# Kernel tuning notes

Measured on AMD Instinct MI355X. Metric: run time of the kernel, lower is better.

Reference implementation:

```python
import jax, jax.numpy as jnp
import numpy as np
from jax import lax

NS, NQ, D, C = 1000, 131072, 1024, 100

def setup_inputs() -> dict:
    key = jax.random.key(0)
    k1, k2, k3, k4 = jax.random.split(key, 4)
    return {
        "support_x": jax.random.normal(k1, (NS, D), dtype=jnp.float32),
        "support_y": jax.random.randint(k2, (NS,), 0, C),
        "query_x": jax.random.normal(k3, (NQ, D), dtype=jnp.float32),
        "query_y": jax.random.randint(k4, (NQ,), 0, C),
        "n_iter": 10,
        "beta": 5,
        "num_classes": C,
    }

def _l2norm(x):
    return x / jnp.linalg.norm(x, axis=1, keepdims=True)

def _sqdist(q, c):
    # ||q - c||^2 = |q|^2 + |c|^2 - 2 q.c   -> [Nq, C]
    q2 = jnp.sum(q * q, axis=1, keepdims=True)
    c2 = jnp.sum(c * c, axis=1)
    return q2 + c2[None, :] - 2.0 * (q @ c.T)

def reference(support_x, support_y, query_x, query_y, n_iter, beta, num_classes):
    betaf = jnp.float32(beta)
    # preprocess_KMeans: sphere by support mean, then L2-normalize
    mean_feature = jnp.mean(support_x, axis=0)
    s = _l2norm(support_x - mean_feature)   # [Ns, D]
    q = _l2norm(query_x - mean_feature)     # [Nq, D]

    # per-class support sums/counts (hard assignments for support points)
    sup_sum = jax.ops.segment_sum(s, support_y, num_segments=num_classes)          # [C, D]
    sup_cnt = jax.ops.segment_sum(jnp.ones((s.shape[0],), s.dtype), support_y,
                                  num_segments=num_classes)                        # [C]
    centroids0 = sup_sum / sup_cnt[:, None]  # class means (intent of original init)

    def step(centroids, _):
        d2 = _sqdist(q, centroids)                       # [Nq, C]
        w = jax.nn.softmax(-betaf * d2, axis=1)          # soft assignment weights
        suma = sup_sum + w.T @ q                         # [C, D]
        sumb = sup_cnt + jnp.sum(w, axis=0)              # [C]
        return suma / sumb[:, None], None

    centroids, _ = lax.scan(step, centroids0, None, length=n_iter)

    pred = jnp.argmin(_sqdist(q, centroids), axis=1)     # nearest centroid
    acc = jnp.mean((pred == query_y).astype(jnp.float32))
    return acc
```

## Files before the change

### kernel.cpp

```cpp
#include <hip/hip_runtime.h>
#include <hip/hip_fp8.h>
#include <math.h>

#define NS 1000
#define NQ 131072
#define D  1024
#define C  100
#define CP 112
#define BETA 5.0f
#define NITER 10
#define KC 64
#define KROWS (NQ/KC)
#define KS8 (KROWS/64)

typedef float f32x4 __attribute__((ext_vector_type(4)));
typedef short s16x8 __attribute__((ext_vector_type(8)));
typedef long s64;
typedef s64 s64x2 __attribute__((ext_vector_type(2)));
typedef unsigned short u16;
typedef unsigned char u8;

__device__ __forceinline__ u16 f2bf(float x) {
  union { float f; unsigned u; } v; v.f = x;
  unsigned r = v.u + 0x7fffu + ((v.u >> 16) & 1u);
  return (u16)(r >> 16);
}
__device__ __forceinline__ float bf2f(u16 h) {
  union { unsigned u; float f; } v; v.u = ((unsigned)h) << 16; return v.f;
}
__device__ __forceinline__ u8 f2fp8(float x) {
  __hip_fp8_e4m3 h(x);
  return (u8)h.__x;
}
__device__ __forceinline__ void gld16(const u16* g, u16* l) {
  __builtin_amdgcn_global_load_lds(
      (const __attribute__((address_space(1))) void*)g,
      (__attribute__((address_space(3))) void*)l, 16, 0, 0);
}
__device__ __forceinline__ void gld16b(const u8* g, u8* l) {
  __builtin_amdgcn_global_load_lds(
      (const __attribute__((address_space(1))) void*)g,
      (__attribute__((address_space(3))) void*)l, 16, 0, 0);
}
__device__ __forceinline__ s16x8 frag32(const u16* plane, int row, int kb) {
  int s = kb ^ (row & 3);
  return *(const s16x8*)(plane + row * 32 + s * 8);
}
__device__ __forceinline__ f32x4 mfma16(s16x8 a, s16x8 b, f32x4 c) {
  return __builtin_amdgcn_mfma_f32_16x16x32_bf16(a, b, c, 0, 0, 0);
}
__device__ __forceinline__ f32x4 mfma8(s64 a, s64 b, f32x4 c) {
  return __builtin_amdgcn_mfma_f32_16x16x32_fp8_fp8(a, b, c, 0, 0, 0);
}


__global__ __launch_bounds__(256) void k_mean(const float* __restrict__ sx,
                                              float* __restrict__ mean) {
  int d = blockIdx.x * 256 + threadIdx.x;
  float a = 0.f;
  for (int r = 0; r < NS; ++r) a += sx[(size_t)r * D + d];
  mean[d] = a / (float)NS;
}

__global__ __launch_bounds__(256) void k_invn(const float* __restrict__ x,
                                              const float* __restrict__ mean,
                                              float* __restrict__ invn) {
  int r = blockIdx.x;
  int t = threadIdx.x;
  float4 v = ((const float4*)(x + (size_t)r * D))[t];
  float4 m = ((const float4*)mean)[t];
  float a = v.x - m.x, b = v.y - m.y, c = v.z - m.z, d = v.w - m.w;
  float s = a * a + b * b + c * c + d * d;
#pragma unroll
  for (int off = 1; off < 64; off <<= 1) s += __shfl_xor(s, off);
  __shared__ float ws[4];
  if ((t & 63) == 0) ws[t >> 6] = s;
  __syncthreads();
  if (t == 0) invn[r] = 1.0f / sqrtf(ws[0] + ws[1] + ws[2] + ws[3]);
}

__global__ __launch_bounds__(256) void k_supsum(const float* __restrict__ sx,
        const int* __restrict__ sy, const float* __restrict__ mean,
        const float* __restrict__ invs, float* __restrict__ supsum,
        float* __restrict__ supcnt) {
  int c = blockIdx.x;
  int t = threadIdx.x;
  float a0 = 0.f, a1 = 0.f, a2 = 0.f, a3 = 0.f;
  int cnt = 0;
  if (c < C) {
    for (int r = 0; r < NS; ++r) {
      if (sy[r] == c) {
        ++cnt;
        float inv = invs[r];
        a0 += (sx[(size_t)r * D + t      ] - mean[t      ]) * inv;
        a1 += (sx[(size_t)r * D + t + 256] - mean[t + 256]) * inv;
        a2 += (sx[(size_t)r * D + t + 512] - mean[t + 512]) * inv;
        a3 += (sx[(size_t)r * D + t + 768] - mean[t + 768]) * inv;
      }
    }
  }
  supsum[(size_t)c * D + t      ] = a0;
  supsum[(size_t)c * D + t + 256] = a1;
  supsum[(size_t)c * D + t + 512] = a2;
  supsum[(size_t)c * D + t + 768] = a3;
  if (t == 0) supcnt[c] = (float)cnt;
}

__global__ void k_zero(int* __restrict__ corr) {
  if (threadIdx.x == 0) corr[0] = 0;
}

__global__ void k_out(const int* __restrict__ corr, float* __restrict__ out) {
  if (threadIdx.x == 0) out[0] = (float)corr[0] * (1.0f / (float)NQ);
}

__global__ __launch_bounds__(256) void k_qsplit(const float* __restrict__ qx,
        const float* __restrict__ mean, const float* __restrict__ invq,
        u16* __restrict__ qfh, u16* __restrict__ qfl,
        u8* __restrict__ qf8, u8* __restrict__ qt8) {
  __shared__ u16 Lh[64][70];
  __shared__ float mloc[64], iloc[64];
  int t = threadIdx.x;
  int q0 = blockIdx.x * 64, d0 = blockIdx.y * 64;
  if (t < 16) ((float4*)mloc)[t] = ((const float4*)(mean + d0))[t];
  else if (t < 32) ((float4*)iloc)[t - 16] = ((const float4*)(invq + q0))[t - 16];
  __syncthreads();
  int r = t >> 2, c0 = (t & 3) * 16;
  float inv = iloc[r];
  const float* src = qx + (size_t)(q0 + r) * D + d0 + c0;
  union { u16 s[16]; uint4 q[2]; } H, L;
  union { u8 b[16]; unsigned long long q[2]; } F;
#pragma unroll
  for (int j = 0; j < 16; j += 4) {
    float4 v = *(const float4*)(src + j);
    float xs[4] = {v.x, v.y, v.z, v.w};
#pragma unroll
    for (int u = 0; u < 4; ++u) {
      float x = (xs[u] - mloc[c0 + j + u]) * inv;
      u16 h = f2bf(x);
      H.s[j + u] = h;
      L.s[j + u] = f2bf(x - bf2f(h));
      F.b[j + u] = f2fp8(16.0f * x);
    }
  }
#pragma unroll
  for (int j = 0; j < 16; j += 2)
    *(ushort2*)&Lh[r][c0 + j] = make_ushort2(H.s[j], H.s[j + 1]);
  {
    int d = d0 + c0;
    int ks = d >> 5;
    int kin = c0 & 16;
    int rowin = (q0 & 64) + r;
    size_t fb = ((size_t)((q0 >> 7) * 32 + ks) * 128 + rowin) * 32 + kin;
    *(uint4*)(qfh + fb)     = H.q[0];
    *(uint4*)(qfh + fb + 8) = H.q[1];
    *(uint4*)(qfl + fb)     = L.q[0];
    *(uint4*)(qfl + fb + 8) = L.q[1];
  }
  {
    int h8 = (c0 >= 32) ? 1 : 0;
    int sA = (c0 & 31) >> 3;
    size_t fb8 = (((size_t)(q0 >> 7) * 16 + (d0 >> 6)) * 8 +
                  ((q0 & 64) >> 4) + (r >> 4)) * 1024;
    int lb = (r & 15) * 16 + h8 * 8;
    *(unsigned long long*)(qf8 + fb8 + sA * 256 + lb)       = F.q[0];
    *(unsigned long long*)(qf8 + fb8 + (sA + 1) * 256 + lb) = F.q[1];
  }
  __syncthreads();
  int tq4 = (t & 15) * 4, td4 = (t >> 4) * 4;
  u16 a[4][4];
#pragma unroll
  for (int i = 0; i < 4; ++i) {
    ushort2 p0 = *(const ushort2*)&Lh[tq4 + i][td4];
    ushort2 p1 = *(const ushort2*)&Lh[tq4 + i][td4 + 2];
    a[i][0] = p0.x; a[i][1] = p0.y; a[i][2] = p1.x; a[i][3] = p1.y;
  }
#pragma unroll
  for (int j = 0; j < 4; ++j) {
    uchar4 o;
    o.x = f2fp8(16.0f * bf2f(a[0][j]));
    o.y = f2fp8(16.0f * bf2f(a[1][j]));
    o.z = f2fp8(16.0f * bf2f(a[2][j]));
    o.w = f2fp8(16.0f * bf2f(a[3][j]));
    *(uchar4*)(qt8 + (size_t)(d0 + td4 + j) * NQ + q0 + tq4) = o;
  }
}

template<int INIT>
__global__ __launch_bounds__(256) void k_updm(const float* __restrict__ supsum,
        const float* __restrict__ part, const float* __restrict__ wsump,
        const float* __restrict__ supcnt,
        u16* __restrict__ cfh, u16* __restrict__ cfl, u8* __restrict__ cf8,
        float* __restrict__ c2) {
  int c = blockIdx.x, t = threadIdx.x;
  __shared__ float red[4];
  float den;
  if (INIT) {
    den = supcnt[c];
  } else {
    float s = 0.f;
    for (int b = t; b < NQ / 128; b += 256) s += wsump[(size_t)b * CP + c];
#pragma unroll
    for (int off = 1; off < 64; off <<= 1) s += __shfl_xor(s, off);
    if ((t & 63) == 0) red[t >> 6] = s;
    __syncthreads();
    den = supcnt[c] + red[0] + red[1] + red[2] + red[3];
    __syncthreads();
  }
  float ss = 0.f;
  float vals[4];
#pragma unroll
  for (int j = 0; j < 4; ++j) {
    int d = t + j * 256;
    float s = supsum[(size_t)c * D + d];
    if (!INIT) {
      float ps = 0.f;
      for (int kc = 0; kc < KC; ++kc) ps += part[((size_t)kc * CP + c) * D + d];
      s += 0.0009765625f * ps;
    }
    float v = (c < C) ? s / den : 0.f;
    vals[j] = v; ss += v * v;
  }
#pragma unroll
  for (int j = 0; j < 4; ++j) {
    int d = t + j * 256;
    size_t a16 = (size_t)(d >> 5) * (CP * 32) + c * 32 +
                 ((((d >> 3) & 3) ^ (c & 3)) * 8) + (d & 7);
    u16 h = f2bf(vals[j]);
    cfh[a16] = h;
    cfl[a16] = f2bf(vals[j] - bf2f(h));
    size_t a8 = ((size_t)(d >> 6) * CP + c) * 64 +
                ((((d >> 4) & 3) ^ (c & 3)) * 16) + (d & 15);
    cf8[a8] = f2fp8(16.0f * vals[j]);
  }
#pragma unroll
  for (int off = 1; off < 64; off <<= 1) ss += __shfl_xor(ss, off);
  __syncthreads();
  if ((t & 63) == 0) red[t >> 6] = ss;
  __syncthreads();
  if (t == 0) c2[c] = (c < C) ? (red[0] + red[1] + red[2] + red[3]) : 1e30f;
}


__global__ __launch_bounds__(256) void k_logits8(
    const u8* __restrict__ qf8, const u8* __restrict__ cf8,
    const float* __restrict__ c2,
    u8* __restrict__ Wf8, float* __restrict__ wsump) {
  __shared__ __align__(16) u8 sm[3 * 7168];
  __shared__ float wred[4][CP];
  int t = threadIdx.x, w = t >> 6, l = t & 63;
  int qblk = blockIdx.x;
  const u8* ap0 = qf8 + (size_t)qblk * 131072 + (size_t)(w * 2) * 1024 + l * 16;
  int s_ = l >> 4, r15 = l & 15;
  int o8 = (s_ & 1) * 8;
  int go0 = s_ >> 1, go1 = 2 + (s_ >> 1);

  f32x4 acc[2][7];
#pragma unroll
  for (int mf = 0; mf < 2; ++mf)
#pragma unroll
    for (int nf = 0; nf < 7; ++nf) acc[mf][nf] = (f32x4){0.f, 0.f, 0.f, 0.f};

  auto stageB = [&](u8* buf, int kb) {
    for (int i = w; i < 7; i += 4)
      gld16b(cf8 + (size_t)kb * 7168 + i * 1024 + l * 16, buf + i * 1024);
  };
  auto computeK = [&](const u8* buf, s64x2 a0, s64x2 a1) {
#pragma unroll
    for (int nf = 0; nf < 7; ++nf) {
      int row = nf * 16 + r15;
      const u8* rp = buf + row * 64;
      int sw = row & 3;
      s64 b0 = *(const s64*)(rp + ((go0 ^ sw) << 4) + o8);
      s64 b1 = *(const s64*)(rp + ((go1 ^ sw) << 4) + o8);
      f32x4 x0 = acc[0][nf], x1 = acc[1][nf];
      x0 = mfma8(a0[0], b0, x0); x0 = mfma8(a0[1], b1, x0);
      x1 = mfma8(a1[0], b0, x1); x1 = mfma8(a1[1], b1, x1);
      acc[0][nf] = x0; acc[1][nf] = x1;
    }
  };
#define WAITC8() { if (w < 3) asm volatile("s_waitcnt vmcnt(4)" ::: "memory"); \
                   else       asm volatile("s_waitcnt vmcnt(3)" ::: "memory"); }

  s64x2 a0A, a1A, a0B, a1B;
  u8 *p0 = sm, *p1 = sm + 7168, *p2 = sm + 14336;
  a0A = *(const s64x2*)ap0; a1A = *(const s64x2*)(ap0 + 1024);
  stageB(p0, 0);
  for (int kp = 0; kp < 8; ++kp) {
    int k = kp * 2;
    { const u8* p = ap0 + (size_t)(k + 1) * 8192;
      a0B = *(const s64x2*)p; a1B = *(const s64x2*)(p + 1024); }
    stageB(p1, k + 1);
    WAITC8();
    __builtin_amdgcn_s_barrier();
    computeK(p0, a0A, a1A);
    if (k + 2 < 16) {
      const u8* p = ap0 + (size_t)(k + 2) * 8192;
      a0A = *(const s64x2*)p; a1A = *(const s64x2*)(p + 1024);
      stageB(p2, k + 2);
      WAITC8();
    } else {
      asm volatile("s_waitcnt vmcnt(0)" ::: "memory");
    }
    __builtin_amdgcn_s_barrier();
    computeK(p1, a0B, a1B);
    u8* tmp = p0; p0 = p2; p2 = p1; p1 = tmp;
  }
  __syncthreads();

  float c2v[7];
#pragma unroll
  for (int nf = 0; nf < 7; ++nf) c2v[nf] = c2[nf * 16 + r15];

  const float LS = 2.0f / 256.0f;
  float wcol[7];
#pragma unroll
  for (int nf = 0; nf < 7; ++nf) wcol[nf] = 0.f;
  u8* Wsh8 = sm;
#pragma unroll
  for (int mf = 0; mf < 2; ++mf)
#pragma unroll
    for (int r = 0; r < 4; ++r) {
      float Lg[7], mx = -INFINITY;
#pragma unroll
      for (int nf = 0; nf < 7; ++nf) {
        Lg[nf] = LS * acc[mf][nf][r] - c2v[nf];
        mx = fmaxf(mx, Lg[nf]);
      }
#pragma unroll
      for (int off = 1; off < 16; off <<= 1) mx = fmaxf(mx, __shfl_xor(mx, off));
      float e[7], s = 0.f;
#pragma unroll
      for (int nf = 0; nf < 7; ++nf) { e[nf] = expf(BETA * (Lg[nf] - mx)); s += e[nf]; }
#pragma unroll
      for (int off = 1; off < 16; off <<= 1) s += __shfl_xor(s, off);
      float is = 1.f / s;
      int qi = w * 32 + mf * 16 + (l >> 4) * 4 + r;
#pragma unroll
      for (int nf = 0; nf < 7; ++nf) {
        float wv = e[nf] * is;
        wcol[nf] += wv;
        int cc = nf * 16 + r15;
        Wsh8[cc * 128 + (((qi >> 4) ^ (cc & 7)) << 4) + (qi & 15)] =
            f2fp8(64.0f * wv);
      }
    }
#pragma unroll
  for (int off = 16; off < 64; off <<= 1)
#pragma unroll
    for (int nf = 0; nf < 7; ++nf) wcol[nf] += __shfl_xor(wcol[nf], off);
  if (l < 16)
#pragma unroll
    for (int nf = 0; nf < 7; ++nf) wred[w][nf * 16 + l] = wcol[nf];
  __syncthreads();
  {
    size_t wb = (size_t)(qblk >> 4) * (32 * 7168);
    int ks0 = (qblk * 2) & 31;
    for (int idx = t; idx < 896; idx += 256) {
      int c = idx >> 3, g = idx & 7;
      uint4 v = *(const uint4*)(Wsh8 + c * 128 + ((g ^ (c & 7)) << 4));
      *(uint4*)(Wf8 + wb + (size_t)(ks0 + (g >> 2)) * 7168 + c * 64 +
                (((g & 3) ^ (c & 3)) << 4)) = v;
    }
  }
  if (t < CP) wsump[(size_t)qblk * CP + t] =
      wred[0][t] + wred[1][t] + wred[2][t] + wred[3][t];
#undef WAITC8
}


__global__ __launch_bounds__(256) void k_wqm8(
    const u8* __restrict__ Wf8, const u8* __restrict__ qt8,
    float* __restrict__ part) {
  __shared__ __align__(16) u8 sm[3][15360];
  int t = threadIdx.x, w = t >> 6, l = t & 63;
  int ck = blockIdx.x;
  int d0 = blockIdx.y * 128;
  size_t wbase = (size_t)ck * (32 * 7168);
  size_t qoff  = (size_t)ck * KROWS;
  int s_ = l >> 4, r15 = l & 15;
  int o8 = (s_ & 1) * 8;
  int go0 = s_ >> 1, go1 = 2 + (s_ >> 1);

  f32x4 acc[7][2];
#pragma unroll
  for (int mf = 0; mf < 7; ++mf)
#pragma unroll
    for (int nf = 0; nf < 2; ++nf) acc[mf][nf] = (f32x4){0.f, 0.f, 0.f, 0.f};

  auto stage = [&](u8* buf, int ks) {
    for (int i = w; i < 7; i += 4)
      gld16b(Wf8 + wbase + (size_t)ks * 7168 + i * 1024 + l * 16, buf + i * 1024);
#pragma unroll
    for (int i2 = w * 2; i2 < w * 2 + 2; ++i2) {
      int row = i2 * 16 + (l >> 2);
      int g = (l & 3) ^ ((l >> 2) & 3);
      gld16b(qt8 + (size_t)(d0 + row) * NQ + qoff + (size_t)ks * 64 + g * 16,
             buf + 7168 + i2 * 1024);
    }
  };
  auto computeK = [&](const u8* buf) {
    const u8* qb = buf + 7168;
    s64 bq00, bq01, bq10, bq11;
    {
      int row = w * 32 + r15;
      const u8* rp = qb + row * 64; int sw = row & 3;
      bq00 = *(const s64*)(rp + ((go0 ^ sw) << 4) + o8);
      bq01 = *(const s64*)(rp + ((go1 ^ sw) << 4) + o8);
    }
    {
      int row = w * 32 + 16 + r15;
      const u8* rp = qb + row * 64; int sw = row & 3;
      bq10 = *(const s64*)(rp + ((go0 ^ sw) << 4) + o8);
      bq11 = *(const s64*)(rp + ((go1 ^ sw) << 4) + o8);
    }
#pragma unroll
    for (int mf = 0; mf < 7; ++mf) {
      int row = mf * 16 + r15;
      const u8* rp = buf + row * 64; int sw = row & 3;
      s64 a0 = *(const s64*)(rp + ((go0 ^ sw) << 4) + o8);
      s64 a1 = *(const s64*)(rp + ((go1 ^ sw) << 4) + o8);
      f32x4 x0 = acc[mf][0], x1 = acc[mf][1];
      x0 = mfma8(a0, bq00, x0); x0 = mfma8(a1, bq01, x0);
      x1 = mfma8(a0, bq10, x1); x1 = mfma8(a1, bq11, x1);
      acc[mf][0] = x0; acc[mf][1] = x1;
    }
  };
#define WAITC4() { if (w < 3) asm volatile("s_waitcnt vmcnt(4)" ::: "memory"); \
                   else       asm volatile("s_waitcnt vmcnt(3)" ::: "memory"); }

  u8 *p0 = sm[0], *p1 = sm[1], *p2 = sm[2];
  stage(p0, 0);
  for (int kp = 0; kp < KS8 / 2; ++kp) {
    int k = kp * 2;
    stage(p1, k + 1);
    WAITC4();
    __builtin_amdgcn_s_barrier();
    computeK(p0);
    if (k + 2 < KS8) {
      stage(p2, k + 2);
      WAITC4();
    } else {
      asm volatile("s_waitcnt vmcnt(0)" ::: "memory");
    }
    __builtin_amdgcn_s_barrier();
    computeK(p1);
    u8* tmp = p0; p0 = p2; p2 = p1; p1 = tmp;
  }
#pragma unroll
  for (int mf = 0; mf < 7; ++mf)
#pragma unroll
    for (int nf = 0; nf < 2; ++nf)
#pragma unroll
      for (int r = 0; r < 4; ++r) {
        int c = mf * 16 + (l >> 4) * 4 + r;
        int dg = d0 + w * 32 + nf * 16 + r15;
        part[((size_t)ck * CP + c) * D + dg] = acc[mf][nf][r];
      }
#undef WAITC4
}


template<int FINAL>
__global__ __launch_bounds__(256) void k_logits(
    const u16* __restrict__ qfh, const u16* __restrict__ qfl,
    const u16* __restrict__ cfh, const u16* __restrict__ cfl,
    const float* __restrict__ c2,
    const int* __restrict__ qy, int* __restrict__ corr) {
  __shared__ __align__(16) u16 sm[3 * 7168];
  int t = threadIdx.x, w = t >> 6, l = t & 63;
  int qblk = blockIdx.x;
  size_t abase = (size_t)qblk * 32 * 128 * 32;
  int aoff = (w * 32 + (l & 15)) * 32 + (l >> 4) * 8;
  int kb = l >> 4;

  f32x4 acc[2][7];
#pragma unroll
  for (int mf = 0; mf < 2; ++mf)
#pragma unroll
    for (int nf = 0; nf < 7; ++nf) acc[mf][nf] = (f32x4){0.f, 0.f, 0.f, 0.f};

#define ALOADQ(ks, H0, H1, L0, L1) { \
    const u16* ap_ = qfh + abase + (size_t)(ks) * 4096 + aoff; \
    H0 = *(const s16x8*)ap_;  H1 = *(const s16x8*)(ap_ + 512); \
    const u16* lp_ = qfl + abase + (size_t)(ks) * 4096 + aoff; \
    L0 = *(const s16x8*)lp_;  L1 = *(const s16x8*)(lp_ + 512); }

  auto stageB = [&](u16* buf, int ks) {
    for (int i = w; i < 14; i += 4) {
      const u16* src = (i < 7) ? (cfh + (size_t)(ks) * 3584 + i * 512 + l * 8)
                               : (cfl + (size_t)(ks) * 3584 + (i - 7) * 512 + l * 8);
      gld16(src, buf + i * 512);
    }
  };
  auto computeK = [&](const u16* buf, s16x8 h0, s16x8 h1, s16x8 l0, s16x8 l1) {
#pragma unroll
    for (int nf = 0; nf < 7; ++nf) {
      int row = nf * 16 + (l & 15);
      s16x8 bh = frag32(buf, row, kb);
      s16x8 bl = frag32(buf + 3584, row, kb);
      f32x4 a0 = acc[0][nf], a1 = acc[1][nf];
      a0 = mfma16(l0, bh, a0); a0 = mfma16(h0, bl, a0); a0 = mfma16(h0, bh, a0);
      a1 = mfma16(l1, bh, a1); a1 = mfma16(h1, bl, a1); a1 = mfma16(h1, bh, a1);
      acc[0][nf] = a0; acc[1][nf] = a1;
    }
  };
#define WAITCF() { if (w < 2) asm volatile("s_waitcnt vmcnt(8)" ::: "memory"); \
                   else       asm volatile("s_waitcnt vmcnt(7)" ::: "memory"); }

  s16x8 h0A = {}, h1A = {}, l0A = {}, l1A = {};
  s16x8 h0B = {}, h1B = {}, l0B = {}, l1B = {};
  u16 *p0 = sm, *p1 = sm + 7168, *p2 = sm + 14336;
  ALOADQ(0, h0A, h1A, l0A, l1A);
  stageB(p0, 0);
  for (int kp = 0; kp < 16; ++kp) {
    int k = kp * 2;
    ALOADQ(k + 1, h0B, h1B, l0B, l1B);
    stageB(p1, k + 1);
    WAITCF();
    __builtin_amdgcn_s_barrier();
    computeK(p0, h0A, h1A, l0A, l1A);
    if (k + 2 < 32) {
      ALOADQ(k + 2, h0A, h1A, l0A, l1A);
      stageB(p2, k + 2);
      WAITCF();
    } else {
      asm volatile("s_waitcnt vmcnt(0)" ::: "memory");
    }
    __builtin_amdgcn_s_barrier();
    computeK(p1, h0B, h1B, l0B, l1B);
    u16* tmp = p0; p0 = p2; p2 = p1; p1 = tmp;
  }
  __syncthreads();

  float c2v[7];
#pragma unroll
  for (int nf = 0; nf < 7; ++nf) c2v[nf] = c2[nf * 16 + (l & 15)];

  int cnt = 0;
#pragma unroll
  for (int mf = 0; mf < 2; ++mf)
#pragma unroll
    for (int r = 0; r < 4; ++r) {
      float bv = -INFINITY; int bi = 0x7fffffff;
#pragma unroll
      for (int nf = 0; nf < 7; ++nf) {
        float Lg = 2.f * acc[mf][nf][r] - c2v[nf];
        int cc = nf * 16 + (l & 15);
        if (Lg > bv || (Lg == bv && cc < bi)) { bv = Lg; bi = cc; }
      }
#pragma unroll
      for (int off = 1; off < 16; off <<= 1) {
        float ov = __shfl_xor(bv, off); int oi = __shfl_xor(bi, off);
        if (ov > bv || (ov == bv && oi < bi)) { bv = ov; bi = oi; }
      }
      if ((l & 15) == 0) {
        int qi = w * 32 + mf * 16 + (l >> 4) * 4 + r;
        cnt += (bi == qy[blockIdx.x * 128 + qi]) ? 1 : 0;
      }
    }
  if ((l & 15) == 0) atomicAdd(corr, cnt);
#undef ALOADQ
#undef WAITCF
}


extern "C" void kernel_launch(void* const* d_in, const int* in_sizes, int n_in,
                              void* d_out, int out_size, void* d_ws, size_t ws_size,
                              hipStream_t stream) {
  const float* sx = (const float*)d_in[0];
  const int*   sy = (const int*)d_in[1];
  const float* qx = (const float*)d_in[2];
  const int*   qy = (const int*)d_in[3];

  char* base = (char*)d_ws;
  size_t o = 0;
  auto take = [&](size_t bytes) { size_t r = o; o += (bytes + 511) & ~(size_t)511; return r; };
  float* mean   = (float*)(base + take(4096));
  float* invs   = (float*)(base + take(4096));
  float* invq   = (float*)(base + take((size_t)NQ * 4));
  float* supsum = (float*)(base + take((size_t)CP * D * 4));
  float* supcnt = (float*)(base + take(512));
  float* c2A    = (float*)(base + take(512));
  float* c2B    = (float*)(base + take(512));
  float* wsump  = (float*)(base + take((size_t)(NQ / 128) * CP * 4));
  int*   corr   = (int*)(base + take(512));
  u16* cfhA = (u16*)(base + take((size_t)CP * D * 2));
  u16* cflA = (u16*)(base + take((size_t)CP * D * 2));
  u16* cfhB = (u16*)(base + take((size_t)CP * D * 2));
  u16* cflB = (u16*)(base + take((size_t)CP * D * 2));
  u8*  cf8A = (u8*)(base + take((size_t)CP * D));
  u8*  cf8B = (u8*)(base + take((size_t)CP * D));
  u8*  Wf8  = (u8*)(base + take((size_t)CP * NQ));
  float* part = (float*)(base + take((size_t)KC * CP * D * 4));
  u16* qfh  = (u16*)(base + take((size_t)NQ * D * 2));
  u16* qfl  = (u16*)(base + take((size_t)NQ * D * 2));
  u8*  qf8  = (u8*)(base + take((size_t)NQ * D));
  u8*  qt8  = (u8*)(base + take((size_t)NQ * D));
  size_t fast_need = o;

  if (ws_size < fast_need) {
    k_zero<<<1, 64, 0, stream>>>((int*)d_out);
    return;
  }

  k_mean<<<dim3(D / 256), 256, 0, stream>>>(sx, mean);
  k_invn<<<dim3(NS), 256, 0, stream>>>(sx, mean, invs);
  k_invn<<<dim3(NQ), 256, 0, stream>>>(qx, mean, invq);
  k_supsum<<<dim3(CP), 256, 0, stream>>>(sx, sy, mean, invs, supsum, supcnt);
  k_updm<1><<<dim3(CP), 256, 0, stream>>>(supsum, part, wsump, supcnt,
                                          cfhA, cflA, cf8A, c2A);
  k_qsplit<<<dim3(NQ / 64, D / 64), 256, 0, stream>>>(qx, mean, invq,
                                                      qfh, qfl, qf8, qt8);

  u16 *chc = cfhA, *clc = cflA, *chn = cfhB, *cln = cflB;
  u8  *c8c = cf8A, *c8n = cf8B;
  float *c2c = c2A, *c2n = c2B;
  for (int it = 0; it < NITER; ++it) {
    k_logits8<<<dim3(NQ / 128), 256, 0, stream>>>(qf8, c8c, c2c, Wf8, wsump);
    k_wqm8<<<dim3(KC, D / 128), 256, 0, stream>>>(Wf8, qt8, part);
    k_updm<0><<<dim3(CP), 256, 0, stream>>>(supsum, part, wsump, supcnt,
                                            chn, cln, c8n, c2n);
    u16* tu;
    tu = chc; chc = chn; chn = tu;
    tu = clc; clc = cln; cln = tu;
    u8* t8 = c8c; c8c = c8n; c8n = t8;
    float* tf = c2c; c2c = c2n; c2n = tf;
  }
  k_zero<<<1, 64, 0, stream>>>(corr);
  k_logits<1><<<dim3(NQ / 128), 256, 0, stream>>>(qfh, qfl, chc, clc, c2c,
                                                  qy, corr);
  k_out<<<1, 64, 0, stream>>>(corr, (float*)d_out);
}
```

Measured before the change: 1.795 ms.

## Fuse query norm into prep, drop bf16 split buffers, split centroid update

The query norm computation moves into a per-64-row prep kernel that writes only the fp8 forward and transposed copies. The bf16 hi/lo query buffers (512 MB written, then read once) are removed; the final logits kernel rebuilds hi/lo on the fly from raw fp32 query rows. The centroid update now runs on a 4x larger grid, with partial squared-norms summed in the consumers. This trades large intermediate writes and an extra pass over the queries for rereading fp32 input and more ALU work in the final kernel.

```diff
diff --git a/kernel.cpp b/kernel.cpp
--- a/kernel.cpp
+++ b/kernel.cpp
@@ -19,6 +19,7 @@
 typedef s64 s64x2 __attribute__((ext_vector_type(2)));
 typedef unsigned short u16;
 typedef unsigned char u8;
+typedef unsigned long long ull;
 
 __device__ __forceinline__ u16 f2bf(float x) {
   union { float f; unsigned u; } v; v.f = x;
@@ -114,75 +115,79 @@
   if (threadIdx.x == 0) out[0] = (float)corr[0] * (1.0f / (float)NQ);
 }
 
-__global__ __launch_bounds__(256) void k_qsplit(const float* __restrict__ qx,
-        const float* __restrict__ mean, const float* __restrict__ invq,
-        u16* __restrict__ qfh, u16* __restrict__ qfl,
+__global__ __launch_bounds__(256) void k_qprep(const float* __restrict__ qx,
+        const float* __restrict__ mean, float* __restrict__ invq,
         u8* __restrict__ qf8, u8* __restrict__ qt8) {
-  __shared__ u16 Lh[64][70];
-  __shared__ float mloc[64], iloc[64];
-  int t = threadIdx.x;
-  int q0 = blockIdx.x * 64, d0 = blockIdx.y * 64;
-  if (t < 16) ((float4*)mloc)[t] = ((const float4*)(mean + d0))[t];
-  else if (t < 32) ((float4*)iloc)[t - 16] = ((const float4*)(invq + q0))[t - 16];
-  __syncthreads();
+  __shared__ float msh[1024];
+  __shared__ float pp[64];
+  __shared__ float invql[64];
+  __shared__ u8 T8[64 * 68];
+  int t = threadIdx.x, w = t >> 6, l = t & 63;
+  int q0 = blockIdx.x * 64;
+  ((float4*)msh)[t] = ((const float4*)mean)[t];
+  __syncthreads();
+
+#pragma unroll 1
+  for (int rr = 0; rr < 16; ++rr) {
+    int row = w * 16 + rr;
+    const float* rp = qx + (size_t)(q0 + row) * D;
+    float s = 0.f;
+#pragma unroll
+    for (int seg = 0; seg < 4; ++seg) {
+      float4 v = *(const float4*)(rp + seg * 256 + l * 4);
+      float4 m = *(const float4*)(msh + seg * 256 + l * 4);
+      float a = v.x - m.x, b = v.y - m.y, c = v.z - m.z, d = v.w - m.w;
+      s += a * a + b * b + c * c + d * d;
+    }
+#pragma unroll
+    for (int off = 1; off < 64; off <<= 1) s += __shfl_xor(s, off);
+    if (l == 0) pp[row] = s;
+  }
+  __syncthreads();
+  if (t < 64) {
+    float iv = 1.0f / sqrtf(pp[t]);
+    invql[t] = iv;
+    invq[q0 + t] = iv;
+  }
+  __syncthreads();
+
   int r = t >> 2, c0 = (t & 3) * 16;
-  float inv = iloc[r];
-  const float* src = qx + (size_t)(q0 + r) * D + d0 + c0;
-  union { u16 s[16]; uint4 q[2]; } H, L;
-  union { u8 b[16]; unsigned long long q[2]; } F;
-#pragma unroll
-  for (int j = 0; j < 16; j += 4) {
-    float4 v = *(const float4*)(src + j);
-    float xs[4] = {v.x, v.y, v.z, v.w};
-#pragma unroll
-    for (int u = 0; u < 4; ++u) {
-      float x = (xs[u] - mloc[c0 + j + u]) * inv;
-      u16 h = f2bf(x);
-      H.s[j + u] = h;
-      L.s[j + u] = f2bf(x - bf2f(h));
-      F.b[j + u] = f2fp8(16.0f * x);
-    }
-  }
-#pragma unroll
-  for (int j = 0; j < 16; j += 2)
-    *(ushort2*)&Lh[r][c0 + j] = make_ushort2(H.s[j], H.s[j + 1]);
-  {
-    int d = d0 + c0;
-    int ks = d >> 5;
-    int kin = c0 & 16;
-    int rowin = (q0 & 64) + r;
-    size_t fb = ((size_t)((q0 >> 7) * 32 + ks) * 128 + rowin) * 32 + kin;
-    *(uint4*)(qfh + fb)     = H.q[0];
-    *(uint4*)(qfh + fb + 8) = H.q[1];
-    *(uint4*)(qfl + fb)     = L.q[0];
-    *(uint4*)(qfl + fb + 8) = L.q[1];
-  }
-  {
-    int h8 = (c0 >= 32) ? 1 : 0;
-    int sA = (c0 & 31) >> 3;
+  float iv = invql[r];
+  int h8 = (c0 >= 32) ? 1 : 0;
+  int sA = (c0 & 31) >> 3;
+  int lb = (r & 15) * 16 + h8 * 8;
+  int tq4 = (t & 15) * 4, td4 = (t >> 4) * 4;
+  for (int d0 = 0; d0 < D; d0 += 64) {
+    const float* src = qx + (size_t)(q0 + r) * D + d0 + c0;
+    union { u8 b[16]; ull q[2]; } F;
+#pragma unroll
+    for (int j = 0; j < 16; j += 4) {
+      float4 v = *(const float4*)(src + j);
+      float xs[4] = {v.x, v.y, v.z, v.w};
+#pragma unroll
+      for (int u = 0; u < 4; ++u) {
+        float x = (xs[u] - msh[d0 + c0 + j + u]) * iv;
+        F.b[j + u] = f2fp8(16.0f * x);
+      }
+    }
     size_t fb8 = (((size_t)(q0 >> 7) * 16 + (d0 >> 6)) * 8 +
                   ((q0 & 64) >> 4) + (r >> 4)) * 1024;
-    int lb = (r & 15) * 16 + h8 * 8;
-    *(unsigned long long*)(qf8 + fb8 + sA * 256 + lb)       = F.q[0];
-    *(unsigned long long*)(qf8 + fb8 + (sA + 1) * 256 + lb) = F.q[1];
-  }
-  __syncthreads();
-  int tq4 = (t & 15) * 4, td4 = (t >> 4) * 4;
-  u16 a[4][4];
-#pragma unroll
-  for (int i = 0; i < 4; ++i) {
-    ushort2 p0 = *(const ushort2*)&Lh[tq4 + i][td4];
-    ushort2 p1 = *(const ushort2*)&Lh[tq4 + i][td4 + 2];
-    a[i][0] = p0.x; a[i][1] = p0.y; a[i][2] = p1.x; a[i][3] = p1.y;
-  }
-#pragma unroll
-  for (int j = 0; j < 4; ++j) {
-    uchar4 o;
-    o.x = f2fp8(16.0f * bf2f(a[0][j]));
-    o.y = f2fp8(16.0f * bf2f(a[1][j]));
-    o.z = f2fp8(16.0f * bf2f(a[2][j]));
-    o.w = f2fp8(16.0f * bf2f(a[3][j]));
-    *(uchar4*)(qt8 + (size_t)(d0 + td4 + j) * NQ + q0 + tq4) = o;
+    *(ull*)(qf8 + fb8 + sA * 256 + lb)       = F.q[0];
+    *(ull*)(qf8 + fb8 + (sA + 1) * 256 + lb) = F.q[1];
+    __syncthreads();
+#pragma unroll
+    for (int j = 0; j < 4; ++j)
+      *(uchar4*)(T8 + r * 68 + c0 + j * 4) =
+          make_uchar4(F.b[j * 4], F.b[j * 4 + 1], F.b[j * 4 + 2], F.b[j * 4 + 3]);
+    __syncthreads();
+    u8 a[4][4];
+#pragma unroll
+    for (int i = 0; i < 4; ++i)
+      *(uchar4*)a[i] = *(const uchar4*)(T8 + (tq4 + i) * 68 + td4);
+#pragma unroll
+    for (int j = 0; j < 4; ++j)
+      *(uchar4*)(qt8 + (size_t)(d0 + td4 + j) * NQ + q0 + tq4) =
+          make_uchar4(a[0][j], a[1][j], a[2][j], a[3][j]);
   }
 }
 
@@ -191,60 +196,58 @@
         const float* __restrict__ part, const float* __restrict__ wsump,
         const float* __restrict__ supcnt,
         u16* __restrict__ cfh, u16* __restrict__ cfl, u8* __restrict__ cf8,
-        float* __restrict__ c2) {
-  int c = blockIdx.x, t = threadIdx.x;
+        float* __restrict__ c2p) {
+  int c = blockIdx.x, by = blockIdx.y, t = threadIdx.x;
   __shared__ float red[4];
   float den;
   if (INIT) {
     den = supcnt[c];
   } else {
     float s = 0.f;
-    for (int b = t; b < NQ / 128; b += 256) s += wsump[(size_t)b * CP + c];
+#pragma unroll
+    for (int b = 0; b < 4; ++b) s += wsump[(size_t)(t + b * 256) * CP + c];
 #pragma unroll
     for (int off = 1; off < 64; off <<= 1) s += __shfl_xor(s, off);
     if ((t & 63) == 0) red[t >> 6] = s;
     __syncthreads();
-    den = supcnt[c] + red[0] + red[1] + red[2] + red[3];
+    den = supcnt[c] + ((red[0] + red[1]) + (red[2] + red[3]));
     __syncthreads();
   }
-  float ss = 0.f;
-  float vals[4];
-#pragma unroll
-  for (int j = 0; j < 4; ++j) {
-    int d = t + j * 256;
-    float s = supsum[(size_t)c * D + d];
-    if (!INIT) {
-      float ps = 0.f;
-      for (int kc = 0; kc < KC; ++kc) ps += part[((size_t)kc * CP + c) * D + d];
-      s += 0.0009765625f * ps;
-    }
-    float v = (c < C) ? s / den : 0.f;
-    vals[j] = v; ss += v * v;
-  }
-#pragma unroll
-  for (int j = 0; j < 4; ++j) {
-    int d = t + j * 256;
-    size_t a16 = (size_t)(d >> 5) * (CP * 32) + c * 32 +
-                 ((((d >> 3) & 3) ^ (c & 3)) * 8) + (d & 7);
-    u16 h = f2bf(vals[j]);
-    cfh[a16] = h;
-    cfl[a16] = f2bf(vals[j] - bf2f(h));
-    size_t a8 = ((size_t)(d >> 6) * CP + c) * 64 +
-                ((((d >> 4) & 3) ^ (c & 3)) * 16) + (d & 15);
-    cf8[a8] = f2fp8(16.0f * vals[j]);
-  }
+  int d = by * 256 + t;
+  float s = supsum[(size_t)c * D + d];
+  if (!INIT) {
+    float p0 = 0.f, p1 = 0.f, p2 = 0.f, p3 = 0.f;
+    for (int kc = 0; kc < KC; kc += 4) {
+      p0 += part[((size_t)(kc + 0) * CP + c) * D + d];
+      p1 += part[((size_t)(kc + 1) * CP + c) * D + d];
+      p2 += part[((size_t)(kc + 2) * CP + c) * D + d];
+      p3 += part[((size_t)(kc + 3) * CP + c) * D + d];
+    }
+    s += 0.0009765625f * ((p0 + p1) + (p2 + p3));
+  }
+  float v = (c < C) ? s / den : 0.f;
+  size_t a16 = (size_t)(d >> 5) * (CP * 32) + c * 32 +
+               ((((d >> 3) & 3) ^ (c & 3)) * 8) + (d & 7);
+  u16 h = f2bf(v);
+  cfh[a16] = h;
+  cfl[a16] = f2bf(v - bf2f(h));
+  size_t a8 = ((size_t)(d >> 6) * CP + c) * 64 +
+              ((((d >> 4) & 3) ^ (c & 3)) * 16) + (d & 15);
+  cf8[a8] = f2fp8(16.0f * v);
+  float ss = v * v;
 #pragma unroll
   for (int off = 1; off < 64; off <<= 1) ss += __shfl_xor(ss, off);
   __syncthreads();
   if ((t & 63) == 0) red[t >> 6] = ss;
   __syncthreads();
-  if (t == 0) c2[c] = (c < C) ? (red[0] + red[1] + red[2] + red[3]) : 1e30f;
+  if (t == 0) c2p[c * 4 + by] =
+      (c < C) ? ((red[0] + red[1]) + (red[2] + red[3])) : 2.5e29f;
 }
 
 
 __global__ __launch_bounds__(256) void k_logits8(
     const u8* __restrict__ qf8, const u8* __restrict__ cf8,
-    const float* __restrict__ c2,
+    const float* __restrict__ c2p,
     u8* __restrict__ Wf8, float* __restrict__ wsump) {
   __shared__ __align__(16) u8 sm[3 * 7168];
   __shared__ float wred[4][CP];
@@ -310,7 +313,11 @@
 
   float c2v[7];
 #pragma unroll
-  for (int nf = 0; nf < 7; ++nf) c2v[nf] = c2[nf * 16 + r15];
+  for (int nf = 0; nf < 7; ++nf) {
+    int cc = nf * 16 + r15;
+    float4 p = *(const float4*)(c2p + cc * 4);
+    c2v[nf] = (p.x + p.y) + (p.z + p.w);
+  }
 
   const float LS = 2.0f / 256.0f;
   float wcol[7];
@@ -461,17 +468,27 @@
 }
 
 
-template<int FINAL>
-__global__ __launch_bounds__(256) void k_logits(
-    const u16* __restrict__ qfh, const u16* __restrict__ qfl,
+__global__ __launch_bounds__(256) void k_final(
+    const float* __restrict__ qx, const float* __restrict__ mean,
+    const float* __restrict__ invq,
     const u16* __restrict__ cfh, const u16* __restrict__ cfl,
-    const float* __restrict__ c2,
+    const float* __restrict__ c2p,
     const int* __restrict__ qy, int* __restrict__ corr) {
   __shared__ __align__(16) u16 sm[3 * 7168];
+  __shared__ float msh[1024];
+  __shared__ float ivsh[128];
   int t = threadIdx.x, w = t >> 6, l = t & 63;
-  int qblk = blockIdx.x;
-  size_t abase = (size_t)qblk * 32 * 128 * 32;
-  int aoff = (w * 32 + (l & 15)) * 32 + (l >> 4) * 8;
+  int q0 = blockIdx.x * 128;
+  ((float4*)msh)[t] = ((const float4*)mean)[t];
+  if (t < 32) ((float4*)ivsh)[t] = ((const float4*)(invq + q0))[t];
+  __syncthreads();
+
+  int r15 = l & 15;
+  int ko = (l >> 4) * 8;
+  int row0 = w * 32 + r15, row1 = row0 + 16;
+  const float* a0p = qx + (size_t)(q0 + row0) * D + ko;
+  const float* a1p = qx + (size_t)(q0 + row1) * D + ko;
+  float iv0 = ivsh[row0], iv1 = ivsh[row1];
   int kb = l >> 4;
 
   f32x4 acc[2][7];
@@ -480,11 +497,11 @@
 #pragma unroll
     for (int nf = 0; nf < 7; ++nf) acc[mf][nf] = (f32x4){0.f, 0.f, 0.f, 0.f};
 
-#define ALOADQ(ks, H0, H1, L0, L1) { \
-    const u16* ap_ = qfh + abase + (size_t)(ks) * 4096 + aoff; \
-    H0 = *(const s16x8*)ap_;  H1 = *(const s16x8*)(ap_ + 512); \
-    const u16* lp_ = qfl + abase + (size_t)(ks) * 4096 + aoff; \
-    L0 = *(const s16x8*)lp_;  L1 = *(const s16x8*)(lp_ + 512); }
+#define ALOADR(ks, R) { \
+    const float* p0_ = a0p + (size_t)(ks) * 32; \
+    const float* p1_ = a1p + (size_t)(ks) * 32; \
+    R[0] = *(const float4*)p0_; R[1] = *(const float4*)(p0_ + 4); \
+    R[2] = *(const float4*)p1_; R[3] = *(const float4*)(p1_ + 4); }
 
   auto stageB = [&](u16* buf, int ks) {
     for (int i = w; i < 14; i += 4) {
@@ -493,10 +510,24 @@
       gld16(src, buf + i * 512);
     }
   };
-  auto computeK = [&](const u16* buf, s16x8 h0, s16x8 h1, s16x8 l0, s16x8 l1) {
+  auto mk = [&](const float4& u0, const float4& u1, float iv, int ks,
+                s16x8& hh, s16x8& ll) {
+    float xs[8] = {u0.x, u0.y, u0.z, u0.w, u1.x, u1.y, u1.z, u1.w};
+#pragma unroll
+    for (int u = 0; u < 8; ++u) {
+      float x = (xs[u] - msh[ks * 32 + ko + u]) * iv;
+      u16 h = f2bf(x);
+      hh[u] = (short)h;
+      ll[u] = (short)f2bf(x - bf2f(h));
+    }
+  };
+  auto computeK = [&](const u16* buf, float4* R, int ks) {
+    s16x8 h0, l0, h1, l1;
+    mk(R[0], R[1], iv0, ks, h0, l0);
+    mk(R[2], R[3], iv1, ks, h1, l1);
 #pragma unroll
     for (int nf = 0; nf < 7; ++nf) {
-      int row = nf * 16 + (l & 15);
+      int row = nf * 16 + r15;
       s16x8 bh = frag32(buf, row, kb);
       s16x8 bl = frag32(buf + 3584, row, kb);
       f32x4 a0 = acc[0][nf], a1 = acc[1][nf];
@@ -508,34 +539,37 @@
 #define WAITCF() { if (w < 2) asm volatile("s_waitcnt vmcnt(8)" ::: "memory"); \
                    else       asm volatile("s_waitcnt vmcnt(7)" ::: "memory"); }
 
-  s16x8 h0A = {}, h1A = {}, l0A = {}, l1A = {};
-  s16x8 h0B = {}, h1B = {}, l0B = {}, l1B = {};
+  float4 rA[4], rB[4];
   u16 *p0 = sm, *p1 = sm + 7168, *p2 = sm + 14336;
-  ALOADQ(0, h0A, h1A, l0A, l1A);
+  ALOADR(0, rA);
   stageB(p0, 0);
   for (int kp = 0; kp < 16; ++kp) {
     int k = kp * 2;
-    ALOADQ(k + 1, h0B, h1B, l0B, l1B);
+    ALOADR(k + 1, rB);
     stageB(p1, k + 1);
     WAITCF();
     __builtin_amdgcn_s_barrier();
-    computeK(p0, h0A, h1A, l0A, l1A);
+    computeK(p0, rA, k);
     if (k + 2 < 32) {
-      ALOADQ(k + 2, h0A, h1A, l0A, l1A);
+      ALOADR(k + 2, rA);
       stageB(p2, k + 2);
       WAITCF();
     } else {
       asm volatile("s_waitcnt vmcnt(0)" ::: "memory");
     }
     __builtin_amdgcn_s_barrier();
-    computeK(p1, h0B, h1B, l0B, l1B);
+    computeK(p1, rB, k + 1);
     u16* tmp = p0; p0 = p2; p2 = p1; p1 = tmp;
   }
   __syncthreads();
 
   float c2v[7];
 #pragma unroll
-  for (int nf = 0; nf < 7; ++nf) c2v[nf] = c2[nf * 16 + (l & 15)];
+  for (int nf = 0; nf < 7; ++nf) {
+    int cc = nf * 16 + r15;
+    float4 p = *(const float4*)(c2p + cc * 4);
+    c2v[nf] = (p.x + p.y) + (p.z + p.w);
+  }
 
   int cnt = 0;
 #pragma unroll
@@ -546,7 +580,7 @@
 #pragma unroll
       for (int nf = 0; nf < 7; ++nf) {
         float Lg = 2.f * acc[mf][nf][r] - c2v[nf];
-        int cc = nf * 16 + (l & 15);
+        int cc = nf * 16 + r15;
         if (Lg > bv || (Lg == bv && cc < bi)) { bv = Lg; bi = cc; }
       }
 #pragma unroll
@@ -554,13 +588,13 @@
         float ov = __shfl_xor(bv, off); int oi = __shfl_xor(bi, off);
         if (ov > bv || (ov == bv && oi < bi)) { bv = ov; bi = oi; }
       }
-      if ((l & 15) == 0) {
+      if (r15 == 0) {
         int qi = w * 32 + mf * 16 + (l >> 4) * 4 + r;
-        cnt += (bi == qy[blockIdx.x * 128 + qi]) ? 1 : 0;
-      }
-    }
-  if ((l & 15) == 0) atomicAdd(corr, cnt);
-#undef ALOADQ
+        cnt += (bi == qy[q0 + qi]) ? 1 : 0;
+      }
+    }
+  if (r15 == 0) atomicAdd(corr, cnt);
+#undef ALOADR
 #undef WAITCF
 }
 
@@ -581,8 +615,8 @@
   float* invq   = (float*)(base + take((size_t)NQ * 4));
   float* supsum = (float*)(base + take((size_t)CP * D * 4));
   float* supcnt = (float*)(base + take(512));
-  float* c2A    = (float*)(base + take(512));
-  float* c2B    = (float*)(base + take(512));
+  float* c2pA   = (float*)(base + take(2048));
+  float* c2pB   = (float*)(base + take(2048));
   float* wsump  = (float*)(base + take((size_t)(NQ / 128) * CP * 4));
   int*   corr   = (int*)(base + take(512));
   u16* cfhA = (u16*)(base + take((size_t)CP * D * 2));
@@ -593,8 +627,6 @@
   u8*  cf8B = (u8*)(base + take((size_t)CP * D));
   u8*  Wf8  = (u8*)(base + take((size_t)CP * NQ));
   float* part = (float*)(base + take((size_t)KC * CP * D * 4));
-  u16* qfh  = (u16*)(base + take((size_t)NQ * D * 2));
-  u16* qfl  = (u16*)(base + take((size_t)NQ * D * 2));
   u8*  qf8  = (u8*)(base + take((size_t)NQ * D));
   u8*  qt8  = (u8*)(base + take((size_t)NQ * D));
   size_t fast_need = o;
@@ -606,21 +638,19 @@
 
   k_mean<<<dim3(D / 256), 256, 0, stream>>>(sx, mean);
   k_invn<<<dim3(NS), 256, 0, stream>>>(sx, mean, invs);
-  k_invn<<<dim3(NQ), 256, 0, stream>>>(qx, mean, invq);
   k_supsum<<<dim3(CP), 256, 0, stream>>>(sx, sy, mean, invs, supsum, supcnt);
-  k_updm<1><<<dim3(CP), 256, 0, stream>>>(supsum, part, wsump, supcnt,
-                                          cfhA, cflA, cf8A, c2A);
-  k_qsplit<<<dim3(NQ / 64, D / 64), 256, 0, stream>>>(qx, mean, invq,
-                                                      qfh, qfl, qf8, qt8);
+  k_updm<1><<<dim3(CP, 4), 256, 0, stream>>>(supsum, part, wsump, supcnt,
+                                             cfhA, cflA, cf8A, c2pA);
+  k_qprep<<<dim3(NQ / 64), 256, 0, stream>>>(qx, mean, invq, qf8, qt8);
 
   u16 *chc = cfhA, *clc = cflA, *chn = cfhB, *cln = cflB;
   u8  *c8c = cf8A, *c8n = cf8B;
-  float *c2c = c2A, *c2n = c2B;
+  float *c2c = c2pA, *c2n = c2pB;
   for (int it = 0; it < NITER; ++it) {
     k_logits8<<<dim3(NQ / 128), 256, 0, stream>>>(qf8, c8c, c2c, Wf8, wsump);
     k_wqm8<<<dim3(KC, D / 128), 256, 0, stream>>>(Wf8, qt8, part);
-    k_updm<0><<<dim3(CP), 256, 0, stream>>>(supsum, part, wsump, supcnt,
-                                            chn, cln, c8n, c2n);
+    k_updm<0><<<dim3(CP, 4), 256, 0, stream>>>(supsum, part, wsump, supcnt,
+                                               chn, cln, c8n, c2n);
     u16* tu;
     tu = chc; chc = chn; chn = tu;
     tu = clc; clc = cln; cln = tu;
@@ -628,7 +658,7 @@
     float* tf = c2c; c2c = c2n; c2n = tf;
   }
   k_zero<<<1, 64, 0, stream>>>(corr);
-  k_logits<1><<<dim3(NQ / 128), 256, 0, stream>>>(qfh, qfl, chc, clc, c2c,
-                                                  qy, corr);
+  k_final<<<dim3(NQ / 128), 256, 0, stream>>>(qx, mean, invq, chc, clc, c2c,
+                                              qy, corr);
   k_out<<<1, 64, 0, stream>>>(corr, (float*)d_out);
 }
```

Result: faster. 1.613 ms (-10.2%).
